# Optimization experiments

Hardware: AMD Instinct MI355X
Metric: run time of the kernel (lower is better)

The kernel has to match this reference:

```python
import jax, jax.numpy as jnp
import numpy as np

N_NODES = 100000
N_EDGES = 1600000
D_IN, D_HID, D_OUT = 256, 512, 48
K_STEPS = 10
ALPHA = 0.1


def setup_inputs() -> dict:
    key = jax.random.key(0)
    k_x, k_e, k_w1, k_w2 = jax.random.split(key, 4)
    x = jax.random.normal(k_x, (N_NODES, D_IN), dtype=jnp.float32)
    edge_index = jax.random.randint(k_e, (2, N_EDGES), 0, N_NODES, dtype=jnp.int64)
    # MLP params (Kaiming-ish scaling)
    W1 = jax.random.normal(k_w1, (D_IN, D_HID), dtype=jnp.float32) * (1.0 / np.sqrt(D_IN))
    b1 = jnp.zeros((D_HID,), dtype=jnp.float32)
    W2 = jax.random.normal(k_w2, (D_HID, D_OUT), dtype=jnp.float32) * (1.0 / np.sqrt(D_HID))
    b2 = jnp.zeros((D_OUT,), dtype=jnp.float32)
    return {"x": x, "edge_index": edge_index, "W1": W1, "b1": b1, "W2": W2, "b2": b2}


def reference(x, edge_index, W1, b1, W2, b2):
    N = x.shape[0]
    # --- MLP encoder ---
    h = jax.nn.relu(x @ W1 + b1) @ W2 + b2  # [N, D_OUT]

    # --- APPNP propagation (PyG defaults: add self-loops, symmetric gcn_norm) ---
    loop = jnp.arange(N, dtype=edge_index.dtype)
    src = jnp.concatenate([edge_index[0], loop])  # [E+N]
    dst = jnp.concatenate([edge_index[1], loop])
    ones = jnp.ones(src.shape[0], dtype=h.dtype)
    deg = jax.ops.segment_sum(ones, dst, num_segments=N)  # in-degree incl. self-loop
    dinv = jnp.where(deg > 0, jax.lax.rsqrt(deg), 0.0)
    norm = dinv[src] * dinv[dst]  # [E+N]

    out = h
    for _ in range(K_STEPS):
        msg = out[src] * norm[:, None]                      # gather + scale
        agg = jax.ops.segment_sum(msg, dst, num_segments=N)  # scatter-add
        out = (1.0 - ALPHA) * agg + ALPHA * h                # teleport mix
    return out
```

## Files before the change

kernel.cpp:

```cpp
#include <hip/hip_runtime.h>
#include <hip/hip_fp16.h>

constexpr int D_IN = 256, D_HID = 512, D_OUT = 48;
constexpr int HPAD = 64;
constexpr int K_STEPS = 10;
constexpr int CAPR = 64;
constexpr int EB   = 4096;

typedef __attribute__((ext_vector_type(8))) __bf16 bf16x8;
typedef __attribute__((ext_vector_type(4))) float f32x4;

__device__ __forceinline__ unsigned short f2bf(float f) {
  unsigned u = __builtin_bit_cast(unsigned, f);
  u += 0x7fffu + ((u >> 16) & 1u);
  return (unsigned short)(u >> 16);
}

__device__ __forceinline__ void gl2lds16(const unsigned short* g, unsigned short* l) {
  __builtin_amdgcn_global_load_lds(
      (const __attribute__((address_space(1))) unsigned int*)g,
      (__attribute__((address_space(3))) unsigned int*)l, 16, 0, 0);
}


__global__ void zero_kernel(int* __restrict__ cnt, int* __restrict__ gcur, int N) {
  int i = blockIdx.x * 256 + threadIdx.x;
  if (i < N) cnt[i] = 0;
  if (blockIdx.x == 0 && threadIdx.x < 256) gcur[threadIdx.x] = 0;
}

__global__ __launch_bounds__(256) void bucket_kernel(
    const int* __restrict__ src, const int* __restrict__ dst,
    int2* __restrict__ fifo, int* __restrict__ gcur, int FCAP, int E) {
  __shared__ int bcnt[256], bbase[256], brank[256];
  int tid = threadIdx.x;
  int e0 = blockIdx.x * EB;
  bcnt[tid] = 0;
  __syncthreads();
  int sv[16], dv[16];
#pragma unroll
  for (int k = 0; k < 16; ++k) {
    int e = e0 + k * 256 + tid;
    if (e < E) {
      dv[k] = __builtin_nontemporal_load(dst + e);
      sv[k] = __builtin_nontemporal_load(src + e);
      atomicAdd(&bcnt[dv[k] >> 9], 1);
    } else {
      dv[k] = -1;
    }
  }
  __syncthreads();
  if (bcnt[tid] > 0) bbase[tid] = atomicAdd(&gcur[tid], bcnt[tid]);
  brank[tid] = 0;
  __syncthreads();
#pragma unroll
  for (int k = 0; k < 16; ++k) {
    if (dv[k] >= 0) {
      int b = dv[k] >> 9;
      int r = atomicAdd(&brank[b], 1);
      fifo[(size_t)b * FCAP + bbase[b] + r] = make_int2(sv[k], dv[k]);
    }
  }
}

__global__ __launch_bounds__(256) void csr_kernel(
    const int2* __restrict__ fifo, const int* __restrict__ gcur,
    int* __restrict__ cnt, int* __restrict__ edges, int FCAP) {
  int b = blockIdx.x;
  int n = gcur[b];
  const int2* f = fifo + (size_t)b * FCAP;
  for (int i = threadIdx.x; i < n; i += 256) {
    int2 v = f[i];
    int r = atomicAdd(&cnt[v.y], 1);
    edges[(size_t)v.y * CAPR + r] = v.x;
  }
}

__global__ void dinvdeg_kernel(const int* __restrict__ cnt, float* __restrict__ dinv,
                               int* __restrict__ pdeg, int N) {
  int n = blockIdx.x * 256 + threadIdx.x;
  if (n < N) {
    int c = cnt[n];
    dinv[n] = rsqrtf((float)(c + 1));
    pdeg[n] = (c + 4) & ~3;
  }
}

__global__ void pad_kernel(const int* __restrict__ cnt, const int* __restrict__ pdeg,
                           int* __restrict__ edges, int N) {
  int n = blockIdx.x * 256 + threadIdx.x;
  if (n >= N) return;
  int a = n * CAPR + cnt[n];
  int b = n * CAPR + pdeg[n];
  edges[a] = n;
  for (int p = a + 1; p < b; ++p) edges[p] = N;
}

__global__ void zrow_kernel(__half* __restrict__ a, __half* __restrict__ b, int N) {
  int t = threadIdx.x;
  a[(size_t)N * HPAD + t] = __float2half(0.f);
  b[(size_t)N * HPAD + t] = __float2half(0.f);
}


__global__ void convert_w1(const float* __restrict__ W1, unsigned short* __restrict__ W1F) {
  int i = blockIdx.x * 256 + threadIdx.x;
  if (i >= D_HID * D_IN) return;
  int c = i >> 8, k = i & 255;
  int ct = c >> 6, tn = (c >> 4) & 3, l15 = c & 15;
  int kb = k >> 5, q = (k >> 3) & 3, j = k & 7;
  int lane = (q << 4) | l15;
  int dst = (((ct * 4 + tn) * 8 + kb) << 9) + lane * 8 + j;
  W1F[dst] = f2bf(W1[k * D_HID + c]);
}

__global__ void convert_w2(const float* __restrict__ W2, unsigned short* __restrict__ W2F) {
  int i = blockIdx.x * 256 + threadIdx.x;
  if (i >= D_OUT * D_HID) return;
  int n = i >> 9, k = i & 511;
  int ct = k >> 6, kk = (k >> 5) & 1, q = (k >> 3) & 3, j = k & 7;
  int tn = n >> 4, l15 = n & 15;
  int lane = (q << 4) | l15;
  int dst = (((ct * 2 + kk) * 3 + tn) << 9) + lane * 8 + j;
  W2F[dst] = f2bf(W2[k * D_OUT + n]);
}


__global__ __launch_bounds__(512, 2) void encoder_kernel(
    const float* __restrict__ x, const float* __restrict__ b1,
    const float* __restrict__ b2, const float* __restrict__ dinvp,
    const unsigned short* __restrict__ W1F,
    const unsigned short* __restrict__ W2F,
    __half* __restrict__ h2, __half* __restrict__ qb, int N) {
  __shared__ unsigned short sW1[2][16384];
  __shared__ unsigned short sHid[8][16][72];
  __shared__ float sB1[512];
  __shared__ float sB2[64];

  int tid = threadIdx.x;
  int w = tid >> 6, lane = tid & 63;
  int q = lane >> 4, l15 = lane & 15;
  int row0 = blockIdx.x * 128 + w * 16;

  auto stageCt = [&](int c, int half) {
    const unsigned short* gsrc = W1F + ((size_t)c << 14) + (w << 9) + lane * 8;
    unsigned short* ldst = &sW1[half][w << 9];
#pragma unroll
    for (int i = 0; i < 4; ++i)
      gl2lds16(gsrc + (i << 12), ldst + (i << 12));
  };

  stageCt(0, 0);
  sB1[tid] = b1[tid];
  if (tid < 48) sB2[tid] = b2[tid];

  int grow = row0 + l15;
  bool rok = grow < N;
  const float* xr = x + (size_t)grow * D_IN;
  float4 xv[16];
#pragma unroll
  for (int jb = 0; jb < 8; ++jb) {
    xv[2 * jb]     = rok ? *(const float4*)(xr + jb * 32 + q * 8)
                         : make_float4(0.f, 0.f, 0.f, 0.f);
    xv[2 * jb + 1] = rok ? *(const float4*)(xr + jb * 32 + q * 8 + 4)
                         : make_float4(0.f, 0.f, 0.f, 0.f);
  }
  uint4 axu[8];
#pragma unroll
  for (int jb = 0; jb < 8; ++jb) {
    union { uint4 u; unsigned short s[8]; } uu;
    float4 v0 = xv[2 * jb], v1 = xv[2 * jb + 1];
    uu.s[0] = f2bf(v0.x); uu.s[1] = f2bf(v0.y); uu.s[2] = f2bf(v0.z); uu.s[3] = f2bf(v0.w);
    uu.s[4] = f2bf(v1.x); uu.s[5] = f2bf(v1.y); uu.s[6] = f2bf(v1.z); uu.s[7] = f2bf(v1.w);
    axu[jb] = uu.u;
  }

  f32x4 hacc[3];
#pragma unroll
  for (int t = 0; t < 3; ++t)
#pragma unroll
    for (int r = 0; r < 4; ++r) hacc[t][r] = 0.f;

  __syncthreads();

  for (int ct = 0; ct < 8; ++ct) {
    int cur = ct & 1;
    if (ct < 7) stageCt(ct + 1, cur ^ 1);

    int c0 = ct * 64;
    f32x4 acc[4];
#pragma unroll
    for (int t = 0; t < 4; ++t)
#pragma unroll
      for (int r = 0; r < 4; ++r) acc[t][r] = 0.f;

    const unsigned short* sb = &sW1[cur][lane * 8];
#pragma unroll
    for (int kb = 0; kb < 8; ++kb) {
      bf16x8 a = __builtin_bit_cast(bf16x8, axu[kb]);
      bf16x8 bq0 = *(const bf16x8*)(sb + (kb << 9));
      bf16x8 bq1 = *(const bf16x8*)(sb + (kb << 9) + 4096);
      bf16x8 bq2 = *(const bf16x8*)(sb + (kb << 9) + 8192);
      bf16x8 bq3 = *(const bf16x8*)(sb + (kb << 9) + 12288);
      acc[0] = __builtin_amdgcn_mfma_f32_16x16x32_bf16(a, bq0, acc[0], 0, 0, 0);
      acc[1] = __builtin_amdgcn_mfma_f32_16x16x32_bf16(a, bq1, acc[1], 0, 0, 0);
      acc[2] = __builtin_amdgcn_mfma_f32_16x16x32_bf16(a, bq2, acc[2], 0, 0, 0);
      acc[3] = __builtin_amdgcn_mfma_f32_16x16x32_bf16(a, bq3, acc[3], 0, 0, 0);
    }
#pragma unroll
    for (int tn = 0; tn < 4; ++tn) {
      int c = tn * 16 + l15;
      float bias = sB1[c0 + c];
#pragma unroll
      for (int rg = 0; rg < 4; ++rg) {
        float v = acc[tn][rg] + bias;
        v = v > 0.f ? v : 0.f;
        sHid[w][q * 4 + rg][c] = f2bf(v);
      }
    }
#pragma unroll
    for (int kk = 0; kk < 2; ++kk) {
      bf16x8 a0 = *(const bf16x8*)&sHid[w][l15][kk * 32 + q * 8];
      const unsigned short* w2b = W2F + (((ct * 2 + kk) * 3) << 9) + lane * 8;
#pragma unroll
      for (int tn = 0; tn < 3; ++tn) {
        bf16x8 b = *(const bf16x8*)(w2b + (tn << 9));
        hacc[tn] = __builtin_amdgcn_mfma_f32_16x16x32_bf16(a0, b, hacc[tn], 0, 0, 0);
      }
    }
    __syncthreads();
  }
  float dv[4];
#pragma unroll
  for (int rg = 0; rg < 4; ++rg) {
    int gr = row0 + q * 4 + rg;
    dv[rg] = (gr < N) ? dinvp[gr] : 0.f;
  }
#pragma unroll
  for (int tn = 0; tn < 3; ++tn) {
    int c = tn * 16 + l15;
    float bias = sB2[c];
#pragma unroll
    for (int rg = 0; rg < 4; ++rg) {
      int gr = row0 + q * 4 + rg;
      if (gr < N) {
        float val = hacc[tn][rg] + bias;
        h2[(size_t)gr * HPAD + c] = __float2half(val);
        qb[(size_t)gr * HPAD + c] = __float2half(dv[rg] * val);
      }
    }
  }
#pragma unroll
  for (int rg = 0; rg < 4; ++rg) {
    int gr = row0 + q * 4 + rg;
    if (gr < N) {
      h2[(size_t)gr * HPAD + 48 + l15] = __float2half(0.f);
      qb[(size_t)gr * HPAD + 48 + l15] = __float2half(0.f);
    }
  }
}


__global__ __launch_bounds__(256) void prop_kernel(
    const __half* __restrict__ cur, const __half* __restrict__ h2,
    const float* __restrict__ dinv, const int* __restrict__ pdeg,
    const int* __restrict__ edges, __half* __restrict__ nxt,
    float* __restrict__ outf, int N, int last) {
  int wid = (blockIdx.x * 256 + threadIdx.x) >> 6;
  int lane = threadIdx.x & 63;
  int half = lane >> 5;
  int slot = (lane >> 3) & 3;
  int s = lane & 7;
  int node = wid * 2 + half;
  bool nok = node < N;
  int p0 = 0, p1 = 0;
  if (nok) { p0 = node * CAPR; p1 = p0 + pdeg[node]; }
  int d = p1 - p0;
  int dmax = max(d, __shfl_xor(d, 32));
  int nb = dmax >> 2;

  float acc[8];
#pragma unroll
  for (int i = 0; i < 8; ++i) acc[i] = 0.f;

  int p = p0 + slot;
  int e0 = N, e1 = N, e2 = N, e3 = N;
  if (nb > 0) e0 = edges[p];
  if (nb > 1) e1 = edges[p + 4];
  if (nb > 2) e2 = edges[p + 8];
  if (nb > 3) e3 = edges[p + 12];
  int b = 0;
  for (; b + 4 <= nb; b += 4) {
    int n0 = N, n1 = N, n2 = N, n3 = N;
    if (b + 4 < nb) n0 = edges[p + 16];
    if (b + 5 < nb) n1 = edges[p + 20];
    if (b + 6 < nb) n2 = edges[p + 24];
    if (b + 7 < nb) n3 = edges[p + 28];
    int i0 = (p      < p1) ? e0 : N;
    int i1 = (p + 4  < p1) ? e1 : N;
    int i2 = (p + 8  < p1) ? e2 : N;
    int i3 = (p + 12 < p1) ? e3 : N;
    union { float4 f; __half2 h[4]; } u0, u1, u2, u3;
    u0.f = *(const float4*)(cur + ((size_t)i0 << 6) + s * 8);
    u1.f = *(const float4*)(cur + ((size_t)i1 << 6) + s * 8);
    u2.f = *(const float4*)(cur + ((size_t)i2 << 6) + s * 8);
    u3.f = *(const float4*)(cur + ((size_t)i3 << 6) + s * 8);
#pragma unroll
    for (int i = 0; i < 4; ++i) {
      float2 f0 = __half22float2(u0.h[i]);
      float2 f1 = __half22float2(u1.h[i]);
      float2 f2 = __half22float2(u2.h[i]);
      float2 f3 = __half22float2(u3.h[i]);
      acc[2 * i]     += (f0.x + f1.x) + (f2.x + f3.x);
      acc[2 * i + 1] += (f0.y + f1.y) + (f2.y + f3.y);
    }
    e0 = n0; e1 = n1; e2 = n2; e3 = n3; p += 16;
  }
  if (b < nb) {
    int i0 = (p < p1) ? e0 : N;
    union { float4 f; __half2 h[4]; } u0;
    u0.f = *(const float4*)(cur + ((size_t)i0 << 6) + s * 8);
#pragma unroll
    for (int i = 0; i < 4; ++i) {
      float2 f0 = __half22float2(u0.h[i]);
      acc[2 * i]     += f0.x;
      acc[2 * i + 1] += f0.y;
    }
  }
  if (b + 1 < nb) {
    int i1 = (p + 4 < p1) ? e1 : N;
    union { float4 f; __half2 h[4]; } u1;
    u1.f = *(const float4*)(cur + ((size_t)i1 << 6) + s * 8);
#pragma unroll
    for (int i = 0; i < 4; ++i) {
      float2 f1 = __half22float2(u1.h[i]);
      acc[2 * i]     += f1.x;
      acc[2 * i + 1] += f1.y;
    }
  }
  if (b + 2 < nb) {
    int i2 = (p + 8 < p1) ? e2 : N;
    union { float4 f; __half2 h[4]; } u2;
    u2.f = *(const float4*)(cur + ((size_t)i2 << 6) + s * 8);
#pragma unroll
    for (int i = 0; i < 4; ++i) {
      float2 f2 = __half22float2(u2.h[i]);
      acc[2 * i]     += f2.x;
      acc[2 * i + 1] += f2.y;
    }
  }
#pragma unroll
  for (int i = 0; i < 8; ++i) {
    acc[i] += __int_as_float(__builtin_amdgcn_ds_swizzle(__float_as_int(acc[i]), 0x201F));
    acc[i] += __int_as_float(__builtin_amdgcn_ds_swizzle(__float_as_int(acc[i]), 0x401F));
  }
  if ((lane & 24) != 0 || !nok) return;
  float di = dinv[node];
  size_t base = ((size_t)node << 6) + s * 8;
  union { float4 f; __half2 h[4]; } uh;
  uh.f = *(const float4*)(h2 + base);
  float outv[8];
#pragma unroll
  for (int i = 0; i < 4; ++i) {
    float2 hf = __half22float2(uh.h[i]);
    outv[2 * i]     = 0.9f * di * acc[2 * i]     + 0.1f * hf.x;
    outv[2 * i + 1] = 0.9f * di * acc[2 * i + 1] + 0.1f * hf.y;
  }
  if (last) {
    if (s < 6) {
      float* op = outf + (size_t)node * D_OUT + s * 8;
      *(float4*)op       = make_float4(outv[0], outv[1], outv[2], outv[3]);
      *(float4*)(op + 4) = make_float4(outv[4], outv[5], outv[6], outv[7]);
    }
  } else {
    union { uint4 u4; __half2 h[4]; } o;
#pragma unroll
    for (int i = 0; i < 4; ++i)
      o.h[i] = __floats2half2_rn(di * outv[2 * i], di * outv[2 * i + 1]);
    *(uint4*)(nxt + base) = o.u4;
  }
}


extern "C" void kernel_launch(void* const* d_in, const int* in_sizes, int n_in,
                              void* d_out, int out_size, void* d_ws, size_t ws_size,
                              hipStream_t stream) {
  (void)n_in; (void)out_size; (void)ws_size;
  const float* x  = (const float*)d_in[0];
  const int*   ei = (const int*)d_in[1];
  const float* W1 = (const float*)d_in[2];
  const float* b1 = (const float*)d_in[3];
  const float* W2 = (const float*)d_in[4];
  const float* b2 = (const float*)d_in[5];
  const int N = in_sizes[0] / D_IN;
  const int E = in_sizes[1] / 2;
  const int* e_src = ei;
  const int* e_dst = ei + E;

  char* ws = (char*)d_ws;
  size_t off = 0;
  auto take = [&](size_t bytes) -> char* {
    char* p = ws + off;
    off += (bytes + 511) & ~(size_t)511;
    return p;
  };
  const int NB2  = (N + 511) >> 9;
  const int FCAP = E / NB2 + 1024;
  int* cnt      = (int*)take((size_t)N * 4);
  float* dinv   = (float*)take((size_t)N * 4);
  int* pdeg     = (int*)take((size_t)N * 4);
  int* gcur     = (int*)take(1024);
  int2* fifo    = (int2*)take((size_t)NB2 * FCAP * 8);
  int* edges    = (int*)take((size_t)N * CAPR * 4 + 1024);
  unsigned short* W1F = (unsigned short*)take((size_t)D_IN * D_HID * 2);
  unsigned short* W2F = (unsigned short*)take((size_t)D_HID * D_OUT * 2);
  __half* h2    = (__half*)take((size_t)N * HPAD * 2);
  __half* bufA  = (__half*)take((size_t)(N + 1) * HPAD * 2);
  __half* bufB  = (__half*)d_out;
  float* outp   = (float*)d_out;

  int nb256 = (N + 255) / 256;
  int ebB   = (E + EB - 1) / EB;

  zero_kernel<<<nb256, 256, 0, stream>>>(cnt, gcur, N);
  bucket_kernel<<<ebB, 256, 0, stream>>>(e_src, e_dst, fifo, gcur, FCAP, E);
  csr_kernel<<<NB2, 256, 0, stream>>>(fifo, gcur, cnt, edges, FCAP);
  dinvdeg_kernel<<<nb256, 256, 0, stream>>>(cnt, dinv, pdeg, N);
  pad_kernel<<<nb256, 256, 0, stream>>>(cnt, pdeg, edges, N);
  zrow_kernel<<<1, 64, 0, stream>>>(bufA, bufB, N);

  convert_w1<<<(D_IN * D_HID + 255) / 256, 256, 0, stream>>>(W1, W1F);
  convert_w2<<<(D_HID * D_OUT + 255) / 256, 256, 0, stream>>>(W2, W2F);
  encoder_kernel<<<(N + 127) / 128, 512, 0, stream>>>(x, b1, b2, dinv, W1F, W2F,
                                                      h2, bufB, N);

  int waves = (N + 1) / 2;
  int pblocks = (waves + 3) / 4;
  const __half* src = bufB;
  __half* dst = bufA;
  for (int it = 1; it <= K_STEPS; ++it) {
    int last = (it == K_STEPS);
    prop_kernel<<<pblocks, 256, 0, stream>>>(src, h2, dinv, pdeg, edges,
                                             dst, outp, N, last);
    src = dst;
    dst = (dst == bufA) ? bufB : bufA;
  }
}
```

Measured before the change: 625.4 us.

## Shrink feature row padding to 48 halves and single-buffer W1 staging

```diff
diff --git a/kernel.cpp b/kernel.cpp
--- a/kernel.cpp
+++ b/kernel.cpp
@@ -2,7 +2,7 @@
 #include <hip/hip_fp16.h>
 
 constexpr int D_IN = 256, D_HID = 512, D_OUT = 48;
-constexpr int HPAD = 64;
+constexpr int HPAD = 48;
 constexpr int K_STEPS = 10;
 constexpr int CAPR = 64;
 constexpr int EB   = 4096;
@@ -98,8 +98,10 @@
 
 __global__ void zrow_kernel(__half* __restrict__ a, __half* __restrict__ b, int N) {
   int t = threadIdx.x;
-  a[(size_t)N * HPAD + t] = __float2half(0.f);
-  b[(size_t)N * HPAD + t] = __float2half(0.f);
+  if (t < HPAD) {
+    a[(size_t)N * HPAD + t] = __float2half(0.f);
+    b[(size_t)N * HPAD + t] = __float2half(0.f);
+  }
 }
 
 
@@ -132,7 +134,7 @@
     const unsigned short* __restrict__ W1F,
     const unsigned short* __restrict__ W2F,
     __half* __restrict__ h2, __half* __restrict__ qb, int N) {
-  __shared__ unsigned short sW1[2][16384];
+  __shared__ unsigned short sW1[16384];
   __shared__ unsigned short sHid[8][16][72];
   __shared__ float sB1[512];
   __shared__ float sB2[64];
@@ -142,15 +144,13 @@
   int q = lane >> 4, l15 = lane & 15;
   int row0 = blockIdx.x * 128 + w * 16;
 
-  auto stageCt = [&](int c, int half) {
-    const unsigned short* gsrc = W1F + ((size_t)c << 14) + (w << 9) + lane * 8;
-    unsigned short* ldst = &sW1[half][w << 9];
+  {
+    const unsigned short* gsrc = W1F + (w << 9) + lane * 8;
+    unsigned short* ldst = &sW1[w << 9];
 #pragma unroll
     for (int i = 0; i < 4; ++i)
       gl2lds16(gsrc + (i << 12), ldst + (i << 12));
-  };
-
-  stageCt(0, 0);
+  }
   sB1[tid] = b1[tid];
   if (tid < 48) sB2[tid] = b2[tid];
 
@@ -184,9 +184,6 @@
   __syncthreads();
 
   for (int ct = 0; ct < 8; ++ct) {
-    int cur = ct & 1;
-    if (ct < 7) stageCt(ct + 1, cur ^ 1);
-
     int c0 = ct * 64;
     f32x4 acc[4];
 #pragma unroll
@@ -194,7 +191,7 @@
 #pragma unroll
       for (int r = 0; r < 4; ++r) acc[t][r] = 0.f;
 
-    const unsigned short* sb = &sW1[cur][lane * 8];
+    const unsigned short* sb = &sW1[lane * 8];
 #pragma unroll
     for (int kb = 0; kb < 8; ++kb) {
       bf16x8 a = __builtin_bit_cast(bf16x8, axu[kb]);
@@ -229,6 +226,14 @@
       }
     }
     __syncthreads();
+    if (ct < 7) {
+      const unsigned short* gsrc = W1F + ((size_t)(ct + 1) << 14) + (w << 9) + lane * 8;
+      unsigned short* ldst = &sW1[w << 9];
+#pragma unroll
+      for (int i = 0; i < 4; ++i)
+        gl2lds16(gsrc + (i << 12), ldst + (i << 12));
+      __syncthreads();
+    }
   }
   float dv[4];
 #pragma unroll
@@ -248,14 +253,6 @@
         h2[(size_t)gr * HPAD + c] = __float2half(val);
         qb[(size_t)gr * HPAD + c] = __float2half(dv[rg] * val);
       }
-    }
-  }
-#pragma unroll
-  for (int rg = 0; rg < 4; ++rg) {
-    int gr = row0 + q * 4 + rg;
-    if (gr < N) {
-      h2[(size_t)gr * HPAD + 48 + l15] = __float2half(0.f);
-      qb[(size_t)gr * HPAD + 48 + l15] = __float2half(0.f);
     }
   }
 }
@@ -271,6 +268,7 @@
   int half = lane >> 5;
   int slot = (lane >> 3) & 3;
   int s = lane & 7;
+  bool sok = s < 6;
   int node = wid * 2 + half;
   bool nok = node < N;
   int p0 = 0, p1 = 0;
@@ -282,6 +280,7 @@
   float acc[8];
 #pragma unroll
   for (int i = 0; i < 8; ++i) acc[i] = 0.f;
+  const float4 zf = make_float4(0.f, 0.f, 0.f, 0.f);
 
   int p = p0 + slot;
   int e0 = N, e1 = N, e2 = N, e3 = N;
@@ -301,10 +300,10 @@
     int i2 = (p + 8  < p1) ? e2 : N;
     int i3 = (p + 12 < p1) ? e3 : N;
     union { float4 f; __half2 h[4]; } u0, u1, u2, u3;
-    u0.f = *(const float4*)(cur + ((size_t)i0 << 6) + s * 8);
-    u1.f = *(const float4*)(cur + ((size_t)i1 << 6) + s * 8);
-    u2.f = *(const float4*)(cur + ((size_t)i2 << 6) + s * 8);
-    u3.f = *(const float4*)(cur + ((size_t)i3 << 6) + s * 8);
+    u0.f = sok ? *(const float4*)(cur + (size_t)i0 * HPAD + s * 8) : zf;
+    u1.f = sok ? *(const float4*)(cur + (size_t)i1 * HPAD + s * 8) : zf;
+    u2.f = sok ? *(const float4*)(cur + (size_t)i2 * HPAD + s * 8) : zf;
+    u3.f = sok ? *(const float4*)(cur + (size_t)i3 * HPAD + s * 8) : zf;
 #pragma unroll
     for (int i = 0; i < 4; ++i) {
       float2 f0 = __half22float2(u0.h[i]);
@@ -319,7 +318,7 @@
   if (b < nb) {
     int i0 = (p < p1) ? e0 : N;
     union { float4 f; __half2 h[4]; } u0;
-    u0.f = *(const float4*)(cur + ((size_t)i0 << 6) + s * 8);
+    u0.f = sok ? *(const float4*)(cur + (size_t)i0 * HPAD + s * 8) : zf;
 #pragma unroll
     for (int i = 0; i < 4; ++i) {
       float2 f0 = __half22float2(u0.h[i]);
@@ -330,7 +329,7 @@
   if (b + 1 < nb) {
     int i1 = (p + 4 < p1) ? e1 : N;
     union { float4 f; __half2 h[4]; } u1;
-    u1.f = *(const float4*)(cur + ((size_t)i1 << 6) + s * 8);
+    u1.f = sok ? *(const float4*)(cur + (size_t)i1 * HPAD + s * 8) : zf;
 #pragma unroll
     for (int i = 0; i < 4; ++i) {
       float2 f1 = __half22float2(u1.h[i]);
@@ -341,7 +340,7 @@
   if (b + 2 < nb) {
     int i2 = (p + 8 < p1) ? e2 : N;
     union { float4 f; __half2 h[4]; } u2;
-    u2.f = *(const float4*)(cur + ((size_t)i2 << 6) + s * 8);
+    u2.f = sok ? *(const float4*)(cur + (size_t)i2 * HPAD + s * 8) : zf;
 #pragma unroll
     for (int i = 0; i < 4; ++i) {
       float2 f2 = __half22float2(u2.h[i]);
@@ -354,9 +353,9 @@
     acc[i] += __int_as_float(__builtin_amdgcn_ds_swizzle(__float_as_int(acc[i]), 0x201F));
     acc[i] += __int_as_float(__builtin_amdgcn_ds_swizzle(__float_as_int(acc[i]), 0x401F));
   }
-  if ((lane & 24) != 0 || !nok) return;
+  if ((lane & 24) != 0 || !nok || !sok) return;
   float di = dinv[node];
-  size_t base = ((size_t)node << 6) + s * 8;
+  size_t base = (size_t)node * HPAD + s * 8;
   union { float4 f; __half2 h[4]; } uh;
   uh.f = *(const float4*)(h2 + base);
   float outv[8];
@@ -367,11 +366,9 @@
     outv[2 * i + 1] = 0.9f * di * acc[2 * i + 1] + 0.1f * hf.y;
   }
   if (last) {
-    if (s < 6) {
-      float* op = outf + (size_t)node * D_OUT + s * 8;
-      *(float4*)op       = make_float4(outv[0], outv[1], outv[2], outv[3]);
-      *(float4*)(op + 4) = make_float4(outv[4], outv[5], outv[6], outv[7]);
-    }
+    float* op = outf + (size_t)node * D_OUT + s * 8;
+    *(float4*)op       = make_float4(outv[0], outv[1], outv[2], outv[3]);
+    *(float4*)(op + 4) = make_float4(outv[4], outv[5], outv[6], outv[7]);
   } else {
     union { uint4 u4; __half2 h[4]; } o;
 #pragma unroll
```

After: 751.6 us. +20.2%, slower.

## Fuse degree and padding kernels; single-buffer W1 tiles in encoder

Applied to the files above, without the earlier changes.

```diff
diff --git a/kernel.cpp b/kernel.cpp
--- a/kernel.cpp
+++ b/kernel.cpp
@@ -76,22 +76,16 @@
   }
 }
 
-__global__ void dinvdeg_kernel(const int* __restrict__ cnt, float* __restrict__ dinv,
-                               int* __restrict__ pdeg, int N) {
-  int n = blockIdx.x * 256 + threadIdx.x;
-  if (n < N) {
-    int c = cnt[n];
-    dinv[n] = rsqrtf((float)(c + 1));
-    pdeg[n] = (c + 4) & ~3;
-  }
-}
-
-__global__ void pad_kernel(const int* __restrict__ cnt, const int* __restrict__ pdeg,
-                           int* __restrict__ edges, int N) {
+__global__ void finish_kernel(const int* __restrict__ cnt, float* __restrict__ dinv,
+                              int* __restrict__ pdeg, int* __restrict__ edges, int N) {
   int n = blockIdx.x * 256 + threadIdx.x;
   if (n >= N) return;
-  int a = n * CAPR + cnt[n];
-  int b = n * CAPR + pdeg[n];
+  int c = cnt[n];
+  dinv[n] = rsqrtf((float)(c + 1));
+  int pd = (c + 4) & ~3;
+  pdeg[n] = pd;
+  int a = n * CAPR + c;
+  int b = n * CAPR + pd;
   edges[a] = n;
   for (int p = a + 1; p < b; ++p) edges[p] = N;
 }
@@ -132,7 +126,7 @@
     const unsigned short* __restrict__ W1F,
     const unsigned short* __restrict__ W2F,
     __half* __restrict__ h2, __half* __restrict__ qb, int N) {
-  __shared__ unsigned short sW1[2][16384];
+  __shared__ unsigned short sW1[16384];
   __shared__ unsigned short sHid[8][16][72];
   __shared__ float sB1[512];
   __shared__ float sB2[64];
@@ -142,15 +136,13 @@
   int q = lane >> 4, l15 = lane & 15;
   int row0 = blockIdx.x * 128 + w * 16;
 
-  auto stageCt = [&](int c, int half) {
-    const unsigned short* gsrc = W1F + ((size_t)c << 14) + (w << 9) + lane * 8;
-    unsigned short* ldst = &sW1[half][w << 9];
+  {
+    const unsigned short* gsrc = W1F + (w << 9) + lane * 8;
+    unsigned short* ldst = &sW1[w << 9];
 #pragma unroll
     for (int i = 0; i < 4; ++i)
       gl2lds16(gsrc + (i << 12), ldst + (i << 12));
-  };
-
-  stageCt(0, 0);
+  }
   sB1[tid] = b1[tid];
   if (tid < 48) sB2[tid] = b2[tid];
 
@@ -184,9 +176,6 @@
   __syncthreads();
 
   for (int ct = 0; ct < 8; ++ct) {
-    int cur = ct & 1;
-    if (ct < 7) stageCt(ct + 1, cur ^ 1);
-
     int c0 = ct * 64;
     f32x4 acc[4];
 #pragma unroll
@@ -194,7 +183,7 @@
 #pragma unroll
       for (int r = 0; r < 4; ++r) acc[t][r] = 0.f;
 
-    const unsigned short* sb = &sW1[cur][lane * 8];
+    const unsigned short* sb = &sW1[lane * 8];
 #pragma unroll
     for (int kb = 0; kb < 8; ++kb) {
       bf16x8 a = __builtin_bit_cast(bf16x8, axu[kb]);
@@ -229,6 +218,14 @@
       }
     }
     __syncthreads();
+    if (ct < 7) {
+      const unsigned short* gsrc = W1F + ((size_t)(ct + 1) << 14) + (w << 9) + lane * 8;
+      unsigned short* ldst = &sW1[w << 9];
+#pragma unroll
+      for (int i = 0; i < 4; ++i)
+        gl2lds16(gsrc + (i << 12), ldst + (i << 12));
+      __syncthreads();
+    }
   }
   float dv[4];
 #pragma unroll
@@ -425,8 +422,7 @@
   zero_kernel<<<nb256, 256, 0, stream>>>(cnt, gcur, N);
   bucket_kernel<<<ebB, 256, 0, stream>>>(e_src, e_dst, fifo, gcur, FCAP, E);
   csr_kernel<<<NB2, 256, 0, stream>>>(fifo, gcur, cnt, edges, FCAP);
-  dinvdeg_kernel<<<nb256, 256, 0, stream>>>(cnt, dinv, pdeg, N);
-  pad_kernel<<<nb256, 256, 0, stream>>>(cnt, pdeg, edges, N);
+  finish_kernel<<<nb256, 256, 0, stream>>>(cnt, dinv, pdeg, edges, N);
   zrow_kernel<<<1, 64, 0, stream>>>(bufA, bufB, N);
 
   convert_w1<<<(D_IN * D_HID + 255) / 256, 256, 0, stream>>>(W1, W1F);
```

After: 606.8 us. 3.0% less time.
